# Performance work log

Measured on AMD Instinct MI355X. Metric: run time of the kernel, lower is better.

Reference implementation:

```python
import jax, jax.numpy as jnp
import numpy as np
from jax import lax

B, T, FEAT = 8, 512, 128
D_MODEL, D_STATE, D_INNER, DT_RANK = 128, 16, 256, 8
N_LAYERS, NUM_CLASSES = 10, 35
FLAT = 64 * (FEAT // 4)  # 2048


def setup_inputs():
    keys = iter(jax.random.split(jax.random.key(0), 48))
    def nrm(shape, s=0.05):
        return jax.random.normal(next(keys), shape, jnp.float32) * s
    inp = {}
    inp['x'] = jax.random.normal(next(keys), (B, T, FEAT), jnp.float32)
    inp['lengths'] = jax.random.randint(next(keys), (B,), 0, T)
    inp['conv_w1'] = nrm((32, 1, 3, 3)); inp['conv_b1'] = nrm((32,))
    inp['bn1_s'] = 1.0 + nrm((32,)); inp['bn1_b'] = nrm((32,))
    inp['conv_w2'] = nrm((32, 32, 3, 3)); inp['conv_b2'] = nrm((32,))
    inp['bn2_s'] = 1.0 + nrm((32,)); inp['bn2_b'] = nrm((32,))
    inp['conv_w3'] = nrm((64, 32, 3, 3)); inp['conv_b3'] = nrm((64,))
    inp['bn3_s'] = 1.0 + nrm((64,)); inp['bn3_b'] = nrm((64,))
    inp['conv_w4'] = nrm((64, 64, 3, 3)); inp['conv_b4'] = nrm((64,))
    inp['bn4_s'] = 1.0 + nrm((64,)); inp['bn4_b'] = nrm((64,))
    inp['proj_w'] = nrm((D_MODEL, FLAT), 0.02); inp['proj_b'] = nrm((D_MODEL,))
    inp['proj_ln_s'] = jnp.ones((D_MODEL,)); inp['proj_ln_b'] = jnp.zeros((D_MODEL,))
    L = N_LAYERS
    inp['blk_ln_s'] = jnp.ones((L, D_MODEL)); inp['blk_ln_b'] = jnp.zeros((L, D_MODEL))
    inp['in_w'] = nrm((L, 2 * D_INNER, D_MODEL))
    inp['cw'] = nrm((L, D_INNER, 4)); inp['cb'] = nrm((L, D_INNER))
    inp['xp_w'] = nrm((L, DT_RANK + 2 * D_STATE, D_INNER))
    inp['dt_w'] = nrm((L, D_INNER, DT_RANK))
    inp['dt_b'] = nrm((L, D_INNER)) - 4.0  # softplus(-4) ~ 0.018: realistic small dt
    inp['A_log'] = jnp.tile(jnp.log(jnp.arange(1, D_STATE + 1, dtype=jnp.float32))[None, None, :], (L, D_INNER, 1))
    inp['Dp'] = jnp.ones((L, D_INNER))
    inp['out_w'] = nrm((L, D_MODEL, D_INNER))
    inp['pre_ln_s'] = jnp.ones((D_MODEL,)); inp['pre_ln_b'] = jnp.zeros((D_MODEL,))
    inp['cls_w1'] = nrm((D_MODEL // 2, D_MODEL)); inp['cls_b1'] = nrm((D_MODEL // 2,))
    inp['cls_w2'] = nrm((NUM_CLASSES, D_MODEL // 2)); inp['cls_b2'] = nrm((NUM_CLASSES,))
    return inp


def _ln(x, s, b):
    m = jnp.mean(x, -1, keepdims=True)
    v = jnp.mean((x - m) ** 2, -1, keepdims=True)
    return (x - m) * lax.rsqrt(v + 1e-5) * s + b


def _conv2d(x, w, b):
    y = lax.conv_general_dilated(x, w, (1, 1), 'SAME', dimension_numbers=('NCHW', 'OIHW', 'NCHW'))
    return y + b[None, :, None, None]


def _bn(x, s, b):  # eval-mode BatchNorm folded to per-channel affine
    return x * s[None, :, None, None] + b[None, :, None, None]


def _pool(x, kh, kw):
    return lax.reduce_window(x, -jnp.inf, lax.max, (1, 1, kh, kw), (1, 1, kh, kw), 'VALID')


def _mamba(x, in_w, cw, cb, xp_w, dt_w, dt_b, A_log, Dp, out_w):
    bb = x.shape[0]
    xz = jnp.einsum('btd,ed->bte', x, in_w)                  # [B,T,2*d_inner]
    xm, z = jnp.split(xz, 2, axis=-1)
    # causal depthwise conv1d (torch pads both sides by 3 then truncates to T == left-pad 3)
    xc = lax.conv_general_dilated(xm.transpose(0, 2, 1), cw[:, None, :], (1,), [(3, 0)],
                                  dimension_numbers=('NCH', 'OIH', 'NCH'), feature_group_count=D_INNER)
    xc = jax.nn.silu(xc + cb[None, :, None]).transpose(0, 2, 1)  # [B,T,d_inner]
    dbc = jnp.einsum('btd,ed->bte', xc, xp_w)
    dt, Bm, Cm = jnp.split(dbc, [DT_RANK, DT_RANK + D_STATE], axis=-1)
    dt = jax.nn.softplus(jnp.einsum('btr,dr->btd', dt, dt_w) + dt_b)  # [B,T,d_inner]
    A = -jnp.exp(A_log)                                      # [d_inner,d_state]
    dA = jnp.exp(dt[..., None] * A)                          # [B,T,d,n]
    dBu = (dt * xc)[..., None] * Bm[:, :, None, :]           # [B,T,d,n]
    def step(h, inp):
        dA_t, dBu_t, C_t = inp
        h = dA_t * h + dBu_t
        return h, jnp.einsum('bdn,bn->bd', h, C_t)
    h0 = jnp.zeros((bb, D_INNER, D_STATE), x.dtype)
    _, ys = lax.scan(step, h0, (dA.transpose(1, 0, 2, 3), dBu.transpose(1, 0, 2, 3), Cm.transpose(1, 0, 2)))
    y = ys.transpose(1, 0, 2) + Dp * xc
    y = y * jax.nn.silu(z)
    return jnp.einsum('btd,ed->bte', y, out_w)


def _forward(x, lengths, conv_w1, conv_b1, bn1_s, bn1_b, conv_w2, conv_b2, bn2_s, bn2_b,
             conv_w3, conv_b3, bn3_s, bn3_b, conv_w4, conv_b4, bn4_s, bn4_b,
             proj_w, proj_b, proj_ln_s, proj_ln_b, blk_ln_s, blk_ln_b,
             in_w, cw, cb, xp_w, dt_w, dt_b, A_log, Dp, out_w,
             pre_ln_s, pre_ln_b, cls_w1, cls_b1, cls_w2, cls_b2):
    h = x.transpose(0, 2, 1)[:, None]                        # [B,1,F,T]
    h = jax.nn.silu(_bn(_conv2d(h, conv_w1, conv_b1), bn1_s, bn1_b))
    h = jax.nn.silu(_bn(_conv2d(h, conv_w2, conv_b2), bn2_s, bn2_b))
    h = _pool(h, 2, 2)
    h = jax.nn.silu(_bn(_conv2d(h, conv_w3, conv_b3), bn3_s, bn3_b))
    h = jax.nn.silu(_bn(_conv2d(h, conv_w4, conv_b4), bn4_s, bn4_b))
    h = _pool(h, 2, 1)                                       # [B,64,F/4,T/2]
    h = h.transpose(0, 3, 1, 2).reshape(h.shape[0], h.shape[3], -1)  # [B,T',64*F/4]
    h = jax.nn.silu(_ln(jnp.einsum('btf,df->btd', h, proj_w) + proj_b, proj_ln_s, proj_ln_b))
    for i in range(N_LAYERS):
        h = h + _mamba(_ln(h, blk_ln_s[i], blk_ln_b[i]), in_w[i], cw[i], cb[i], xp_w[i],
                       dt_w[i], dt_b[i], A_log[i], Dp[i], out_w[i])
    h = _ln(h, pre_ln_s, pre_ln_b)
    t_lens = jnp.clip(lengths // 2, 1)
    mask = (jnp.arange(h.shape[1])[None, :] < t_lens[:, None]).astype(h.dtype)[..., None]
    pooled = (h * mask).sum(1) / jnp.clip(mask.sum(1), 1.0)
    c = jax.nn.silu(jnp.einsum('bd,hd->bh', pooled, cls_w1) + cls_b1)
    return jnp.einsum('bh,ch->bc', c, cls_w2) + cls_b2


def reference(x, lengths, conv_w1, conv_b1, bn1_s, bn1_b, conv_w2, conv_b2, bn2_s, bn2_b,
              conv_w3, conv_b3, bn3_s, bn3_b, conv_w4, conv_b4, bn4_s, bn4_b,
              proj_w, proj_b, proj_ln_s, proj_ln_b, blk_ln_s, blk_ln_b,
              in_w, cw, cb, xp_w, dt_w, dt_b, A_log, Dp, out_w,
              pre_ln_s, pre_ln_b, cls_w1, cls_b1, cls_w2, cls_b2):
    return _forward(x, lengths, conv_w1, conv_b1, bn1_s, bn1_b, conv_w2, conv_b2, bn2_s, bn2_b,
                    conv_w3, conv_b3, bn3_s, bn3_b, conv_w4, conv_b4, bn4_s, bn4_b,
                    proj_w, proj_b, proj_ln_s, proj_ln_b, blk_ln_s, blk_ln_b,
                    in_w, cw, cb, xp_w, dt_w, dt_b, A_log, Dp, out_w,
                    pre_ln_s, pre_ln_b, cls_w1, cls_b1, cls_w2, cls_b2)
```

## Files before the change

kernel.cpp:

```cpp
#include <hip/hip_runtime.h>
#include <math.h>

#define B_ 8
#define T_ 512
#define FEAT_ 128
#define TP 256
#define DM 128
#define DI 256
#define DS 16
#define DTR 8
#define NL 10

__device__ __forceinline__ float fsilu(float x){ return x / (1.f + __expf(-x)); }
__device__ __forceinline__ float fsoftplus(float x){ return (x > 20.f) ? x : log1pf(__expf(x)); }

__global__ void k_transpose_x(const float* __restrict__ x, float* __restrict__ xT){
  int idx = blockIdx.x*256 + threadIdx.x;
  if(idx >= B_*FEAT_*T_) return;
  int t = idx % T_; int f = (idx/T_) % FEAT_; int b = idx/(T_*FEAT_);
  xT[idx] = x[((size_t)b*T_ + t)*FEAT_ + f];
}

__device__ __forceinline__ void wt_one(const float* __restrict__ w, float* __restrict__ o,
                                       int idx, int CO, int CIN){
  int k = idx % 9; int ci = (idx/9) % CIN; int co = idx/(9*CIN);
  o[((size_t)(ci*(CO>>3) + (co>>3)))*72 + (co&7)*9 + k] = w[idx];
}
__global__ void k_wt_all(const float* __restrict__ w1, const float* __restrict__ w2,
                         const float* __restrict__ w3, const float* __restrict__ w4,
                         float* __restrict__ o1, float* __restrict__ o2,
                         float* __restrict__ o3, float* __restrict__ o4){
  int idx = blockIdx.x*256 + threadIdx.x;
  if(idx < 288){ wt_one(w1, o1, idx, 32, 1); return; }
  idx -= 288;
  if(idx < 9216){ wt_one(w2, o2, idx, 32, 32); return; }
  idx -= 9216;
  if(idx < 18432){ wt_one(w3, o3, idx, 64, 32); return; }
  idx -= 18432;
  if(idx < 36864){ wt_one(w4, o4, idx, 64, 64); return; }
}

template<int CIN, int CO, int CPW, int CIG, int COG>
__global__ __launch_bounds__(256) void k_conv_t5(const float* __restrict__ in,
     const float* __restrict__ wt, const float* __restrict__ cb,
     const float* __restrict__ bs, const float* __restrict__ bb,
     float* __restrict__ out, int H, int W){
  constexpr int NS = CO/CPW;
  __shared__ __align__(16) float tile[CIG*360];
  int tid = threadIdx.x;
  int lane = tid & 63;
  int wav = __builtin_amdgcn_readfirstlane(tid >> 6);
  int wpr = W >> 4, hpr = H >> 4;
  int idx = blockIdx.x;
  int cog = idx % COG; idx /= COG;
  int tj = idx % wpr; idx /= wpr;
  int ti = idx % hpr; int b = idx / hpr;
  int i0 = ti*16, j0 = tj*16;
  int r = lane & 15, cg = lane >> 4;
  int wslot = cog*4 + wav;
  const float* wbase = wt + (size_t)wslot*72;
  float acc[CPW][4] = {};
  for(int cig = 0; cig < CIN; cig += CIG){
    __syncthreads();
    for(int u = tid; u < CIG*324; u += 256){
      int ci = u / 324; int rem = u - ci*324; int rr = rem / 18; int cc = rem - rr*18;
      int gi = i0 - 1 + rr, gj = j0 - 1 + cc;
      float v = 0.f;
      if(gi >= 0 && gi < H && gj >= 0 && gj < W)
        v = in[((size_t)(b*CIN + cig + ci)*H + gi)*W + gj];
      tile[ci*360 + rr*20 + cc] = v;
    }
    __syncthreads();
    for(int ci = 0; ci < CIG; ci++){
      const float4* wp4 = (const float4*)(wbase + (size_t)(cig+ci)*(NS*72));
      float4 w4q[18];
      #pragma unroll
      for(int q=0;q<18;q++) w4q[q] = wp4[q];
      const float* wf = (const float*)w4q;
      #pragma unroll
      for(int kh=0;kh<3;kh++){
        float4 a = *(const float4*)&tile[ci*360 + (r+kh)*20 + cg*4];
        float4 bv = *(const float4*)&tile[ci*360 + (r+kh)*20 + cg*4 + 4];
        float v[6] = {a.x,a.y,a.z,a.w,bv.x,bv.y};
        #pragma unroll
        for(int co=0;co<CPW;co++){
          #pragma unroll
          for(int kw=0;kw<3;kw++){
            float wv = wf[co*9 + kh*3 + kw];
            #pragma unroll
            for(int u2=0;u2<4;u2++)
              acc[co][u2] = fmaf(wv, v[kw+u2], acc[co][u2]);
          }
        }
      }
    }
  }
  int i = i0 + r;
  #pragma unroll
  for(int co=0; co<CPW; co++){
    int c = cog*(4*CPW) + wav*CPW + co;
    float s = bs[c], bias = cb[c]*s + bb[c];
    float4 o;
    o.x = fsilu(acc[co][0]*s + bias);
    o.y = fsilu(acc[co][1]*s + bias);
    o.z = fsilu(acc[co][2]*s + bias);
    o.w = fsilu(acc[co][3]*s + bias);
    *(float4*)&out[((size_t)(b*CO + c)*H + i)*W + j0 + cg*4] = o;
  }
}

__global__ void k_pool2x2(const float* __restrict__ in, float* __restrict__ out,
                          int C, int Hi, int Wi){
  int Ho = Hi>>1, Wo = Wi>>1;
  int total = B_*C*Ho*Wo;
  int idx = blockIdx.x*256 + threadIdx.x;
  if(idx >= total) return;
  int j = idx % Wo; int i = (idx/Wo)%Ho; int c = (idx/(Wo*Ho))%C; int b = idx/(Wo*Ho*C);
  const float* p = in + (((size_t)(b*C+c)*Hi + 2*i)*Wi + 2*j);
  out[idx] = fmaxf(fmaxf(p[0], p[1]), fmaxf(p[Wi], p[Wi+1]));
}

__global__ __launch_bounds__(256) void k_proj(const float* __restrict__ R0,
    const float* __restrict__ W, float* __restrict__ pbuf){
  __shared__ __align__(16) float As[16][33];
  __shared__ __align__(16) float Ws[16][68];
  int tid = threadIdx.x;
  int n0 = blockIdx.x*64, m0 = blockIdx.y*32;
  int kc = blockIdx.z;
  int b = m0 >> 8;
  int t_base = m0 & 255;
  int tx = tid&15, ty = tid>>4;
  float acc[2][4] = {};
  for(int k0=0; k0<256; k0+=16){
    int kg0 = kc*256 + k0;
    if(tid < 128){
      int row = tid>>2, cq = (tid&3)*4;
      #pragma unroll
      for(int c2=0;c2<4;c2++){
        int k = kg0 + cq + c2;
        int c = k>>5, hh = k&31;
        const float* p = R0 + (((size_t)(b*64+c)*64 + 2*hh)*256 + t_base + row);
        As[cq+c2][row] = fmaxf(p[0], p[256]);
      }
    } else {
      int u = tid - 128; int n = u>>1, cq = (u&1)*8;
      const float* wp = W + (size_t)(n0+n)*2048 + kg0 + cq;
      float4 v0 = *(const float4*)wp, v1 = *(const float4*)(wp+4);
      Ws[cq+0][n]=v0.x; Ws[cq+1][n]=v0.y; Ws[cq+2][n]=v0.z; Ws[cq+3][n]=v0.w;
      Ws[cq+4][n]=v1.x; Ws[cq+5][n]=v1.y; Ws[cq+6][n]=v1.z; Ws[cq+7][n]=v1.w;
    }
    __syncthreads();
    #pragma unroll
    for(int kk=0;kk<16;kk++){
      float a0 = As[kk][ty*2+0];
      float a1 = As[kk][ty*2+1];
      float4 w4 = *(const float4*)&Ws[kk][tx*4];
      float wv4[4] = {w4.x,w4.y,w4.z,w4.w};
      #pragma unroll
      for(int j=0;j<4;j++){
        acc[0][j] = fmaf(a0, wv4[j], acc[0][j]);
        acc[1][j] = fmaf(a1, wv4[j], acc[1][j]);
      }
    }
    __syncthreads();
  }
  float* pb = pbuf + (size_t)kc*2048*DM;
  #pragma unroll
  for(int iu=0;iu<2;iu++){
    int m = m0 + ty*2 + iu;
    #pragma unroll
    for(int j=0;j<4;j++){
      int n = n0 + tx*4 + j;
      pb[(size_t)m*DM + n] = acc[iu][j];
    }
  }
}

__global__ void k_lnp(const float* __restrict__ pbuf, const float* __restrict__ bias,
                      const float* __restrict__ g, const float* __restrict__ b,
                      float* __restrict__ out){
  int row = blockIdx.x;
  int t = threadIdx.x;
  float v0 = bias[t], v1 = bias[t+64];
  #pragma unroll
  for(int kc=0;kc<8;kc++){
    const float* p = pbuf + ((size_t)kc*2048 + row)*DM;
    v0 += p[t]; v1 += p[t+64];
  }
  float s = v0 + v1;
  #pragma unroll
  for(int m=32;m>=1;m>>=1) s += __shfl_xor(s, m);
  float mean = s * (1.f/128.f);
  float e0 = v0-mean, e1 = v1-mean;
  float q = e0*e0 + e1*e1;
  #pragma unroll
  for(int m=32;m>=1;m>>=1) q += __shfl_xor(q, m);
  float inv = rsqrtf(q*(1.f/128.f) + 1e-5f);
  float o0 = fsilu(e0*inv*g[t] + b[t]);
  float o1 = fsilu(e1*inv*g[t+64] + b[t+64]);
  float* po = out + (size_t)row*DM;
  po[t] = o0; po[t+64] = o1;
}

template<int SILU>
__global__ void k_ln(const float* __restrict__ in, const float* __restrict__ g,
                     const float* __restrict__ b, float* __restrict__ out){
  int row = blockIdx.x;
  int t = threadIdx.x;
  const float* p = in + (size_t)row*DM;
  float v0 = p[t], v1 = p[t+64];
  float s = v0 + v1;
  #pragma unroll
  for(int m=32;m>=1;m>>=1) s += __shfl_xor(s, m);
  float mean = s * (1.f/128.f);
  float e0 = v0-mean, e1 = v1-mean;
  float q = e0*e0 + e1*e1;
  #pragma unroll
  for(int m=32;m>=1;m>>=1) q += __shfl_xor(q, m);
  float inv = rsqrtf(q*(1.f/128.f) + 1e-5f);
  float o0 = e0*inv*g[t] + b[t];
  float o1 = e1*inv*g[t+64] + b[t+64];
  if(SILU){ o0 = fsilu(o0); o1 = fsilu(o1); }
  float* po = out + (size_t)row*DM;
  po[t] = o0; po[t+64] = o1;
}

__global__ __launch_bounds__(256) void k_lnxz(const float* __restrict__ hbuf,
    const float* __restrict__ g, const float* __restrict__ bb,
    const float* __restrict__ W, float* __restrict__ out){
  __shared__ __align__(16) float lns[32][132];
  __shared__ __align__(16) float Ws[16][68];
  int tid = threadIdx.x;
  int n0 = blockIdx.x*64, m0 = blockIdx.y*32;
  for(int u=tid; u<1024; u+=256){
    int row = u>>5, c4 = (u&31)*4;
    float4 v = *(const float4*)(hbuf + (size_t)(m0+row)*DM + c4);
    lns[row][c4] = v.x; lns[row][c4+1] = v.y; lns[row][c4+2] = v.z; lns[row][c4+3] = v.w;
  }
  __syncthreads();
  {
    int lane = tid & 63, wv = tid >> 6;
    for(int rr = wv; rr < 32; rr += 4){
      float v0 = lns[rr][lane], v1 = lns[rr][lane+64];
      float s = v0+v1;
      #pragma unroll
      for(int mm=32;mm>=1;mm>>=1) s += __shfl_xor(s,mm);
      float mean = s*(1.f/128.f);
      float e0 = v0-mean, e1 = v1-mean;
      float q = e0*e0+e1*e1;
      #pragma unroll
      for(int mm=32;mm>=1;mm>>=1) q += __shfl_xor(q,mm);
      float inv = rsqrtf(q*(1.f/128.f)+1e-5f);
      lns[rr][lane]    = e0*inv*g[lane] + bb[lane];
      lns[rr][lane+64] = e1*inv*g[lane+64] + bb[lane+64];
    }
  }
  __syncthreads();
  int tx = tid&15, ty = tid>>4;
  float acc[2][4] = {};
  for(int k0=0;k0<128;k0+=16){
    {
      int n = tid>>2, c4 = (tid&3)*4;
      float4 v = *(const float4*)(W + (size_t)(n0+n)*DM + k0 + c4);
      Ws[c4+0][n]=v.x; Ws[c4+1][n]=v.y; Ws[c4+2][n]=v.z; Ws[c4+3][n]=v.w;
    }
    __syncthreads();
    #pragma unroll
    for(int kk=0;kk<16;kk++){
      float a0 = lns[ty*2+0][k0+kk];
      float a1 = lns[ty*2+1][k0+kk];
      float4 w4 = *(const float4*)&Ws[kk][tx*4];
      float wv4[4] = {w4.x,w4.y,w4.z,w4.w};
      #pragma unroll
      for(int j=0;j<4;j++){
        acc[0][j] = fmaf(a0, wv4[j], acc[0][j]);
        acc[1][j] = fmaf(a1, wv4[j], acc[1][j]);
      }
    }
    __syncthreads();
  }
  #pragma unroll
  for(int iu=0;iu<2;iu++){
    int m = m0 + ty*2 + iu;
    float* po = out + (size_t)m*512 + n0 + tx*4;
    #pragma unroll
    for(int j=0;j<4;j++) po[j] = acc[iu][j];
  }
}

__global__ __launch_bounds__(256) void k_xproj8(const float* __restrict__ xz,
    const float* __restrict__ cw, const float* __restrict__ cb,
    const float* __restrict__ xpw, const float* __restrict__ dtw,
    const float* __restrict__ dtb_, float* __restrict__ xc_g,
    float* __restrict__ dbc_g, float* __restrict__ dt_g){
  __shared__ float xzs[11][64];
  __shared__ float As[64][9];
  __shared__ float Wp[64][41];
  __shared__ float dtin[8][9];
  __shared__ float dtw_s[256][9];
  int tid = threadIdx.x;
  int row0 = blockIdx.x*8; int b = row0 >> 8; int t0 = row0 & 255;
  int rA = tid & 7, cgA = tid >> 3;
  int dlC = tid & 63, rqC = tid >> 6;
  float acc0 = 0.f, acc1 = 0.f;
  for(int ch=0; ch<4; ch++){
    int d0 = ch*64;
    __syncthreads();
    for(int u=tid; u<11*64; u+=256){
      int rr = u>>6, dl = u&63;
      int t = t0 + rr - 3;
      xzs[rr][dl] = (t >= 0) ? xz[((size_t)(b*TP)+t)*512 + d0 + dl] : 0.f;
    }
    for(int u=tid; u<40*64; u+=256){
      int nn = u>>6, dk = u&63;
      Wp[dk][nn] = xpw[(size_t)nn*DI + d0 + dk];
    }
    __syncthreads();
    {
      float cw0 = cw[(d0+dlC)*4+0], cw1 = cw[(d0+dlC)*4+1];
      float cw2 = cw[(d0+dlC)*4+2], cw3 = cw[(d0+dlC)*4+3];
      float cbv = cb[d0+dlC];
      #pragma unroll
      for(int i=0;i<2;i++){
        int rr = rqC*2 + i;
        float a = cbv;
        a = fmaf(cw0, xzs[rr+0][dlC], a);
        a = fmaf(cw1, xzs[rr+1][dlC], a);
        a = fmaf(cw2, xzs[rr+2][dlC], a);
        a = fmaf(cw3, xzs[rr+3][dlC], a);
        float v = fsilu(a);
        As[dlC][rr] = v;
        xc_g[((size_t)row0 + rr)*DI + d0 + dlC] = v;
      }
    }
    __syncthreads();
    for(int dk=0; dk<64; dk++){
      float a = As[dk][rA];
      acc0 = fmaf(a, Wp[dk][cgA], acc0);
      if(cgA < 8) acc1 = fmaf(a, Wp[dk][cgA+32], acc1);
    }
  }
  if(cgA < 8){
    dtin[rA][cgA] = acc0;
    dbc_g[((size_t)row0 + rA)*40 + cgA + 32] = acc1;
  } else {
    dbc_g[((size_t)row0 + rA)*40 + cgA] = acc0;
  }
  for(int u=tid; u<256*8; u+=256) dtw_s[u>>3][u&7] = dtw[u];
  __syncthreads();
  {
    int d = tid;
    float bias = dtb_[d];
    float w8[8];
    #pragma unroll
    for(int k=0;k<8;k++) w8[k] = dtw_s[d][k];
    #pragma unroll
    for(int r2=0;r2<8;r2++){
      float a = bias;
      #pragma unroll
      for(int k=0;k<8;k++) a = fmaf(dtin[r2][k], w8[k], a);
      dt_g[((size_t)row0 + r2)*DI + d] = fsoftplus(a);
    }
  }
}

__global__ __launch_bounds__(1024) void k_scan3(const float* __restrict__ dtb,
      const float* __restrict__ xc, const float* __restrict__ xz,
      const float* __restrict__ dbc, const float* __restrict__ A_log,
      const float* __restrict__ Dp, float* __restrict__ y){
  __shared__ float dt_s[TP][8], xc_s[TP][8];
  __shared__ float Bs[TP][16], Cs[TP][16];
  __shared__ float Eb[8][128], Pb[8][128];
  int tid = threadIdx.x;
  int c = tid >> 7, gl = (tid >> 4) & 7, n = tid & 15;
  int dblk = blockIdx.x & 31, b = blockIdx.x >> 5;
  int d0 = dblk*8;
  size_t rbase = (size_t)b*TP;
  for(int u=tid; u<TP*8; u+=1024){
    int tt = u>>3, gg = u&7;
    size_t r = rbase + tt;
    dt_s[tt][gg] = dtb[r*DI + d0 + gg];
    xc_s[tt][gg] = xc [r*DI + d0 + gg];
  }
  for(int u=tid; u<TP*16; u+=1024){
    int tt = u>>4, nn = u&15;
    size_t r = rbase + tt;
    Bs[tt][nn] = dbc[r*40 + 8  + nn];
    Cs[tt][nn] = dbc[r*40 + 24 + nn];
  }
  __syncthreads();
  int d = d0 + gl;
  float An = -__expf(A_log[d*DS + n]);
  float h = 0.f, dtsum = 0.f;
  int tA = c*32;
  float yloc[32], ev[32];
  #pragma unroll
  for(int i=0;i<32;i++){
    int t = tA + i;
    float dtv = dt_s[t][gl];
    dtsum += dtv;
    float e = __expf(dtv*An);
    ev[i] = e;
    h = fmaf(e, h, dtv*xc_s[t][gl]*Bs[t][n]);
    float p = h*Cs[t][n];
    p += __shfl_xor(p,1); p += __shfl_xor(p,2);
    p += __shfl_xor(p,4); p += __shfl_xor(p,8);
    yloc[i] = p;
  }
  Eb[c][gl*16+n] = h;
  Pb[c][gl*16+n] = __expf(An*dtsum);
  __syncthreads();
  float g = 0.f;
  for(int cp=0; cp<c; cp++)
    g = fmaf(Pb[cp][gl*16+n], g, Eb[cp][gl*16+n]);
  float Dpd = Dp[d];
  #pragma unroll
  for(int i=0;i<32;i++){
    int t = tA + i;
    g *= ev[i];
    float p = g*Cs[t][n];
    p += __shfl_xor(p,1); p += __shfl_xor(p,2);
    p += __shfl_xor(p,4); p += __shfl_xor(p,8);
    if(n==0){
      float zv = xz[(rbase+t)*512 + DI + d];
      float xcv = xc_s[t][gl];
      y[(rbase+t)*DI + d] = (yloc[i] + p + Dpd*xcv) * fsilu(zv);
    }
  }
}

__global__ __launch_bounds__(256) void k_out16(const float* __restrict__ A,
    const float* __restrict__ W, float* __restrict__ C){
  __shared__ float As[16][17];
  __shared__ __align__(16) float Ws[16][68];
  int tid = threadIdx.x;
  int n0 = blockIdx.x*64, m0 = blockIdx.y*16;
  int tx = tid&15, ty = tid>>4;
  float acc[4] = {};
  for(int k0=0;k0<256;k0+=16){
    {
      int row = tid>>4, kk = tid&15;
      As[kk][row] = A[(size_t)(m0+row)*DI + k0 + kk];
    }
    {
      int n = tid>>2, cq = (tid&3)*4;
      float4 v = *(const float4*)(W + (size_t)(n0+n)*DI + k0 + cq);
      Ws[cq+0][n]=v.x; Ws[cq+1][n]=v.y; Ws[cq+2][n]=v.z; Ws[cq+3][n]=v.w;
    }
    __syncthreads();
    #pragma unroll
    for(int kk=0;kk<16;kk++){
      float a0 = As[kk][ty];
      float4 w4 = *(const float4*)&Ws[kk][tx*4];
      acc[0] = fmaf(a0, w4.x, acc[0]);
      acc[1] = fmaf(a0, w4.y, acc[1]);
      acc[2] = fmaf(a0, w4.z, acc[2]);
      acc[3] = fmaf(a0, w4.w, acc[3]);
    }
    __syncthreads();
  }
  int m = m0 + ty;
  float* cp = &C[(size_t)m*DM + n0 + tx*4];
  cp[0] += acc[0]; cp[1] += acc[1]; cp[2] += acc[2]; cp[3] += acc[3];
}

__global__ void k_head(const float* __restrict__ hln, const int* __restrict__ lengths,
                       const float* __restrict__ w1, const float* __restrict__ b1,
                       const float* __restrict__ w2, const float* __restrict__ b2,
                       float* __restrict__ out){
  __shared__ float pooled[DM];
  __shared__ float cbuf[64];
  int b = blockIdx.x, tid = threadIdx.x;
  int tl = lengths[b] >> 1; if(tl < 1) tl = 1;
  float s = 0.f;
  const float* p = hln + (size_t)b*TP*DM + tid;
  for(int t=0;t<tl;t++) s += p[(size_t)t*DM];
  pooled[tid] = s / (float)tl;
  __syncthreads();
  if(tid < 64){
    float a = b1[tid];
    const float* wp = w1 + tid*DM;
    for(int k=0;k<DM;k++) a = fmaf(pooled[k], wp[k], a);
    cbuf[tid] = fsilu(a);
  }
  __syncthreads();
  if(tid < 35){
    float a = b2[tid];
    const float* wp = w2 + tid*64;
    for(int k=0;k<64;k++) a = fmaf(cbuf[k], wp[k], a);
    out[b*35+tid] = a;
  }
}

extern "C" void kernel_launch(void* const* d_in, const int* in_sizes, int n_in,
                              void* d_out, int out_size, void* d_ws, size_t ws_size,
                              hipStream_t stream){
  (void)in_sizes; (void)n_in; (void)out_size; (void)ws_size;
  const float* x        = (const float*)d_in[0];
  const int*   lengths  = (const int*)  d_in[1];
  const float* conv_w1  = (const float*)d_in[2];  const float* conv_b1 = (const float*)d_in[3];
  const float* bn1_s    = (const float*)d_in[4];  const float* bn1_b   = (const float*)d_in[5];
  const float* conv_w2  = (const float*)d_in[6];  const float* conv_b2 = (const float*)d_in[7];
  const float* bn2_s    = (const float*)d_in[8];  const float* bn2_b   = (const float*)d_in[9];
  const float* conv_w3  = (const float*)d_in[10]; const float* conv_b3 = (const float*)d_in[11];
  const float* bn3_s    = (const float*)d_in[12]; const float* bn3_b   = (const float*)d_in[13];
  const float* conv_w4  = (const float*)d_in[14]; const float* conv_b4 = (const float*)d_in[15];
  const float* bn4_s    = (const float*)d_in[16]; const float* bn4_b   = (const float*)d_in[17];
  const float* proj_w   = (const float*)d_in[18]; const float* proj_b  = (const float*)d_in[19];
  const float* proj_ln_s= (const float*)d_in[20]; const float* proj_ln_b=(const float*)d_in[21];
  const float* blk_ln_s = (const float*)d_in[22]; const float* blk_ln_b =(const float*)d_in[23];
  const float* in_w     = (const float*)d_in[24];
  const float* cw       = (const float*)d_in[25]; const float* cbv     = (const float*)d_in[26];
  const float* xp_w     = (const float*)d_in[27];
  const float* dt_w     = (const float*)d_in[28]; const float* dt_b    = (const float*)d_in[29];
  const float* A_log    = (const float*)d_in[30]; const float* Dp      = (const float*)d_in[31];
  const float* out_w    = (const float*)d_in[32];
  const float* pre_ln_s = (const float*)d_in[33]; const float* pre_ln_b= (const float*)d_in[34];
  const float* cls_w1   = (const float*)d_in[35]; const float* cls_b1  = (const float*)d_in[36];
  const float* cls_w2   = (const float*)d_in[37]; const float* cls_b2  = (const float*)d_in[38];

  float* ws   = (float*)d_ws;
  float* R0   = ws;
  float* R1   = R0 + 16777216;
  float* xT   = R1 + 16777216;
  float* hbuf = xT + 524288;
  float* lnb  = hbuf + 262144;
  float* xzb  = lnb + 262144;
  float* xcb  = xzb + 1048576;
  float* dbcb = xcb + 524288;
  float* dtbb = dbcb + 81920;
  float* yb   = dtbb + 524288;
  float* wt1  = yb + 524288;
  float* wt2  = wt1 + 288;
  float* wt3  = wt2 + 9216;
  float* wt4  = wt3 + 18432;

  k_wt_all<<<254, 256, 0, stream>>>(conv_w1, conv_w2, conv_w3, conv_w4, wt1, wt2, wt3, wt4);

  k_transpose_x<<<2048, 256, 0, stream>>>(x, xT);
  k_conv_t5<1,32,8,1,1><<<8*8*32, 256, 0, stream>>>(xT, wt1, conv_b1, bn1_s, bn1_b, R0, 128, 512);
  k_conv_t5<32,32,8,32,1><<<8*8*32, 256, 0, stream>>>(R0, wt2, conv_b2, bn2_s, bn2_b, R1, 128, 512);
  k_pool2x2<<<(8*32*64*256)/256, 256, 0, stream>>>(R1, R0, 32, 128, 512);
  k_conv_t5<32,64,8,32,2><<<8*4*16*2, 256, 0, stream>>>(R0, wt3, conv_b3, bn3_s, bn3_b, R1, 64, 256);
  k_conv_t5<64,64,8,32,2><<<8*4*16*2, 256, 0, stream>>>(R1, wt4, conv_b4, bn4_s, bn4_b, R0, 64, 256);

  {
    dim3 gd(2, 64, 8);
    k_proj<<<gd, 256, 0, stream>>>(R0, proj_w, R1);
  }
  k_lnp<<<2048, 64, 0, stream>>>(R1, proj_b, proj_ln_s, proj_ln_b, hbuf);

  for(int i=0;i<NL;i++){
    { dim3 gd(8, 64);
      k_lnxz<<<gd, 256, 0, stream>>>(hbuf, blk_ln_s + i*DM, blk_ln_b + i*DM,
                                     in_w + (size_t)i*512*DM, xzb); }
    k_xproj8<<<256, 256, 0, stream>>>(xzb, cw + (size_t)i*DI*4, cbv + i*DI,
                                      xp_w + (size_t)i*40*DI, dt_w + (size_t)i*DI*DTR,
                                      dt_b + i*DI, xcb, dbcb, dtbb);
    k_scan3<<<256, 1024, 0, stream>>>(dtbb, xcb, xzb, dbcb, A_log + (size_t)i*DI*DS, Dp + i*DI, yb);
    { dim3 gd(2, 128);
      k_out16<<<gd, 256, 0, stream>>>(yb, out_w + (size_t)i*DM*DI, hbuf); }
  }

  k_ln<0><<<2048, 64, 0, stream>>>(hbuf, pre_ln_s, pre_ln_b, lnb);
  k_head<<<8, 128, 0, stream>>>(lnb, lengths, cls_w1, cls_b1, cls_w2, cls_b2, (float*)d_out);
}
```

Baseline: 1.340 ms.

## Reorder conv weights to co-innermost layout and shrink input-channel tile to 8

Conv weights are now stored per wave slot as [ci][k][8 co], so each 3x3 tap loads two float4 vectors holding all eight output channels. Before, all 72 weights per input channel were preloaded into 18 float4 registers. The inner loop is restructured to iterate over the nine taps with the input rows held in registers. The shared-memory input tile is reduced from 32 to 8 channels, which lowers LDS use per block and may raise occupancy, at the cost of more sync/reload rounds.

Result: no change. 1.317 ms (-1.7%).

```diff
diff --git a/kernel.cpp b/kernel.cpp
--- a/kernel.cpp
+++ b/kernel.cpp
@@ -24,7 +24,7 @@
 __device__ __forceinline__ void wt_one(const float* __restrict__ w, float* __restrict__ o,
                                        int idx, int CO, int CIN){
   int k = idx % 9; int ci = (idx/9) % CIN; int co = idx/(9*CIN);
-  o[((size_t)(ci*(CO>>3) + (co>>3)))*72 + (co&7)*9 + k] = w[idx];
+  o[((size_t)(((co>>3)*CIN + ci)*9 + k))*8 + (co&7)] = w[idx];
 }
 __global__ void k_wt_all(const float* __restrict__ w1, const float* __restrict__ w2,
                          const float* __restrict__ w3, const float* __restrict__ w4,
@@ -41,11 +41,11 @@
 }
 
 template<int CIN, int CO, int CPW, int CIG, int COG>
-__global__ __launch_bounds__(256) void k_conv_t5(const float* __restrict__ in,
+__global__ __launch_bounds__(256) void k_conv_t6(const float* __restrict__ in,
      const float* __restrict__ wt, const float* __restrict__ cb,
      const float* __restrict__ bs, const float* __restrict__ bb,
      float* __restrict__ out, int H, int W){
-  constexpr int NS = CO/CPW;
+  static_assert(CPW == 8, "CPW must be 8");
   __shared__ __align__(16) float tile[CIG*360];
   int tid = threadIdx.x;
   int lane = tid & 63;
@@ -58,7 +58,7 @@
   int i0 = ti*16, j0 = tj*16;
   int r = lane & 15, cg = lane >> 4;
   int wslot = cog*4 + wav;
-  const float* wbase = wt + (size_t)wslot*72;
+  const float* wbase = wt + (size_t)wslot*(CIN*72);
   float acc[CPW][4] = {};
   for(int cig = 0; cig < CIN; cig += CIG){
     __syncthreads();
@@ -72,25 +72,26 @@
     }
     __syncthreads();
     for(int ci = 0; ci < CIG; ci++){
-      const float4* wp4 = (const float4*)(wbase + (size_t)(cig+ci)*(NS*72));
-      float4 w4q[18];
-      #pragma unroll
-      for(int q=0;q<18;q++) w4q[q] = wp4[q];
-      const float* wf = (const float*)w4q;
+      float v[3][6];
       #pragma unroll
       for(int kh=0;kh<3;kh++){
         float4 a = *(const float4*)&tile[ci*360 + (r+kh)*20 + cg*4];
         float4 bv = *(const float4*)&tile[ci*360 + (r+kh)*20 + cg*4 + 4];
-        float v[6] = {a.x,a.y,a.z,a.w,bv.x,bv.y};
+        v[kh][0]=a.x; v[kh][1]=a.y; v[kh][2]=a.z; v[kh][3]=a.w;
+        v[kh][4]=bv.x; v[kh][5]=bv.y;
+      }
+      const float* wci = wbase + (size_t)(cig+ci)*72;
+      #pragma unroll
+      for(int k9=0;k9<9;k9++){
+        int kh = k9/3, kw = k9%3;
+        float4 wA = *(const float4*)(wci + k9*8);
+        float4 wB = *(const float4*)(wci + k9*8 + 4);
+        float wv[8] = {wA.x,wA.y,wA.z,wA.w,wB.x,wB.y,wB.z,wB.w};
         #pragma unroll
-        for(int co=0;co<CPW;co++){
+        for(int co=0;co<8;co++){
           #pragma unroll
-          for(int kw=0;kw<3;kw++){
-            float wv = wf[co*9 + kh*3 + kw];
-            #pragma unroll
-            for(int u2=0;u2<4;u2++)
-              acc[co][u2] = fmaf(wv, v[kw+u2], acc[co][u2]);
-          }
+          for(int u2=0;u2<4;u2++)
+            acc[co][u2] = fmaf(wv[co], v[kh][kw+u2], acc[co][u2]);
         }
       }
     }
@@ -538,11 +539,11 @@
   k_wt_all<<<254, 256, 0, stream>>>(conv_w1, conv_w2, conv_w3, conv_w4, wt1, wt2, wt3, wt4);
 
   k_transpose_x<<<2048, 256, 0, stream>>>(x, xT);
-  k_conv_t5<1,32,8,1,1><<<8*8*32, 256, 0, stream>>>(xT, wt1, conv_b1, bn1_s, bn1_b, R0, 128, 512);
-  k_conv_t5<32,32,8,32,1><<<8*8*32, 256, 0, stream>>>(R0, wt2, conv_b2, bn2_s, bn2_b, R1, 128, 512);
+  k_conv_t6<1,32,8,1,1><<<8*8*32, 256, 0, stream>>>(xT, wt1, conv_b1, bn1_s, bn1_b, R0, 128, 512);
+  k_conv_t6<32,32,8,8,1><<<8*8*32, 256, 0, stream>>>(R0, wt2, conv_b2, bn2_s, bn2_b, R1, 128, 512);
   k_pool2x2<<<(8*32*64*256)/256, 256, 0, stream>>>(R1, R0, 32, 128, 512);
-  k_conv_t5<32,64,8,32,2><<<8*4*16*2, 256, 0, stream>>>(R0, wt3, conv_b3, bn3_s, bn3_b, R1, 64, 256);
-  k_conv_t5<64,64,8,32,2><<<8*4*16*2, 256, 0, stream>>>(R1, wt4, conv_b4, bn4_s, bn4_b, R0, 64, 256);
+  k_conv_t6<32,64,8,8,2><<<8*4*16*2, 256, 0, stream>>>(R0, wt3, conv_b3, bn3_s, bn3_b, R1, 64, 256);
+  k_conv_t6<64,64,8,8,2><<<8*4*16*2, 256, 0, stream>>>(R1, wt4, conv_b4, bn4_s, bn4_b, R0, 64, 256);
 
   {
     dim3 gd(2, 64, 8);
```
